# Performance work log

Hardware: AMD Instinct MI355X
Metric: run time of the kernel (lower is better)

The kernel has to match this reference:

```python
import jax, jax.numpy as jnp
import numpy as np

INPUT_DIM = 1024
EMBED_DIM = 256


def setup_inputs() -> dict:
    key = jax.random.key(0)
    ks = jax.random.split(key, 7)
    s_in = 1.0 / np.sqrt(INPUT_DIM)
    x = jax.random.normal(ks[0], (4, 2048, INPUT_DIM), dtype=jnp.float32)
    Wq = jax.random.uniform(ks[1], (INPUT_DIM, EMBED_DIM), jnp.float32, -s_in, s_in)
    bq = jax.random.uniform(ks[2], (EMBED_DIM,), jnp.float32, -s_in, s_in)
    Wk = jax.random.uniform(ks[3], (INPUT_DIM, EMBED_DIM), jnp.float32, -s_in, s_in)
    bk = jax.random.uniform(ks[4], (EMBED_DIM,), jnp.float32, -s_in, s_in)
    Wv = jax.random.uniform(ks[5], (INPUT_DIM, EMBED_DIM), jnp.float32, -s_in, s_in)
    bv = jax.random.uniform(ks[6], (EMBED_DIM,), jnp.float32, -s_in, s_in)
    return {"x": x, "Wq": Wq, "bq": bq, "Wk": Wk, "bk": bk, "Wv": Wv, "bv": bv}


def reference(x, Wq, bq, Wk, bk, Wv, bv):
    # B,T,C -> single-head attention. NOTE: original multiplies by C**0.5.
    C = x.shape[-1]
    scale = jnp.asarray(C, x.dtype) ** 0.5
    q = jnp.einsum('btc,ce->bte', x, Wq) + bq  # [B,T,E]
    k = jnp.einsum('btc,ce->bte', x, Wk) + bk
    v = jnp.einsum('btc,ce->bte', x, Wv) + bv
    wei = jnp.einsum('bqe,bke->bqk', q, k) * scale  # [B,T,T]
    wei = jax.nn.softmax(wei, axis=-1)
    # dropout p=0.0 (eval): identity
    out = jnp.einsum('bqk,bke->bqe', wei, v)  # [B,T,E]
    return out
```

## Files before the change

kernel.cpp:

```cpp
#include <hip/hip_runtime.h>
#include <math.h>

#define IDIM 1024
#define EDIM 256
#define NB 4
#define NT 2048
#define NROW 8192

typedef __attribute__((ext_vector_type(8))) short short8;
typedef __attribute__((ext_vector_type(4))) float f32x4;

#define MFMA16(A,B,C) __builtin_amdgcn_mfma_f32_16x16x32_bf16(A,B,C,0,0,0)
#define GLD16(gsrc, ldst) __builtin_amdgcn_global_load_lds( \
    (const __attribute__((address_space(1))) unsigned int*)(gsrc), \
    (__attribute__((address_space(3))) unsigned int*)(ldst), 16, 0, 0)

#define WAITV4() asm volatile("s_waitcnt vmcnt(4)" ::: "memory")
#define WAITV0() asm volatile("s_waitcnt vmcnt(0)" ::: "memory")
#define BAR() do { asm volatile("" ::: "memory"); __builtin_amdgcn_s_barrier(); \
                   asm volatile("" ::: "memory"); } while (0)

__device__ __forceinline__ unsigned short f2bf(float x){
    unsigned u = __builtin_bit_cast(unsigned, x);
    u += 0x7fffu + ((u >> 16) & 1u);
    return (unsigned short)(u >> 16);
}
__device__ __forceinline__ float bf2f(unsigned short h){
    unsigned u = ((unsigned)h) << 16;
    return __builtin_bit_cast(float, u);
}

__global__ __launch_bounds__(256) void split_w(
    const float* __restrict__ Wq, const float* __restrict__ Wk, const float* __restrict__ Wv,
    ushort* __restrict__ Wqh, ushort* __restrict__ Wql,
    ushort* __restrict__ Wkh, ushort* __restrict__ Wkl,
    ushort* __restrict__ Wvh)
{
    int u = blockIdx.x * 256 + threadIdx.x;
    int z   = u >> 15;
    int rem = u & 32767;
    int ko  = rem >> 8;
    int e   = rem & 255;
    const float* W = (z == 0) ? Wq : (z == 1) ? Wk : Wv;
    ushort* Oh = (z == 0) ? Wqh : (z == 1) ? Wkh : Wvh;
    ushort* Ol = (z == 0) ? Wql : Wkl;
    union { ushort us[8]; uint4 v; } hi, lo;
    #pragma unroll
    for (int j = 0; j < 8; ++j) {
        float wv = W[(size_t)(ko * 8 + j) * 256 + e];
        unsigned short h = f2bf(wv);
        hi.us[j] = h;
        lo.us[j] = f2bf(wv - bf2f(h));
    }
    *(uint4*)(Oh + (size_t)e * 1024 + ko * 8) = hi.v;
    if (z < 2) *(uint4*)(Ol + (size_t)e * 1024 + ko * 8) = lo.v;
}

__global__ __launch_bounds__(256) void qkv_proj(
    const float* __restrict__ X,
    const ushort* __restrict__ Whq, const ushort* __restrict__ Wlq,
    const ushort* __restrict__ Whk, const ushort* __restrict__ Wlk,
    const ushort* __restrict__ Whv,
    const float* __restrict__ bq, const float* __restrict__ bk, const float* __restrict__ bv,
    ushort* __restrict__ Qh, ushort* __restrict__ Ql,
    ushort* __restrict__ Kh, ushort* __restrict__ Kl,
    ushort* __restrict__ Vt)
{
    __shared__ ushort Ah[2][259 * 8], Al[2][259 * 8];
    __shared__ ushort Bh[2][512 * 8], Bl[2][512 * 8];

    const int tid = threadIdx.x;
    const int lane = tid & 63, w = tid >> 6;
    const int ln = tid & 15, quad = (tid >> 4) & 3;
    const int z = blockIdx.z;
    const int n0 = blockIdx.x * 128, m0 = blockIdx.y * 64;
    const ushort* Wh = (z == 0) ? Whq : (z == 1) ? Whk : Whv;
    const ushort* Wl = (z == 0) ? Wlq : Wlk;

    f32x4 acc[4][2];
    #pragma unroll
    for (int mi = 0; mi < 4; ++mi)
        #pragma unroll
        for (int ni = 0; ni < 2; ++ni) acc[mi][ni] = (f32x4){0.f, 0.f, 0.f, 0.f};

    const int am = tid >> 2, ak8 = (tid & 3) * 8;
    const int unit = (tid & 3) * 65 + am;
    const float* xp = X + (size_t)(m0 + am) * IDIM + ak8;
    const ushort* bsrc0 = Wh + (size_t)(n0 + lane) * IDIM + w * 8;
    const ushort* bsrc1 = Wh + (size_t)(n0 + 64 + lane) * IDIM + w * 8;
    const ushort* blsrc0 = Wl + (size_t)(n0 + lane) * IDIM + w * 8;
    const ushort* blsrc1 = Wl + (size_t)(n0 + 64 + lane) * IDIM + w * 8;

#define QSTAGE(pb, kk) do { \
    GLD16(bsrc0 + (kk), Bh[pb] + w * 1024); \
    GLD16(bsrc1 + (kk), Bh[pb] + w * 1024 + 512); \
    if (z < 2) { GLD16(blsrc0 + (kk), Bl[pb] + w * 1024); \
                 GLD16(blsrc1 + (kk), Bl[pb] + w * 1024 + 512); } \
    float4 a0 = *(const float4*)(xp + (kk)); \
    float4 a1 = *(const float4*)(xp + (kk) + 4); \
    float xv[8] = {a0.x, a0.y, a0.z, a0.w, a1.x, a1.y, a1.z, a1.w}; \
    union { ushort us[8]; uint4 v; } hi, lo; \
    _Pragma("unroll") \
    for (int j = 0; j < 8; ++j) { \
        unsigned short hh = f2bf(xv[j]); \
        hi.us[j] = hh; \
        lo.us[j] = f2bf(xv[j] - bf2f(hh)); \
    } \
    *(uint4*)(Ah[pb] + unit * 8) = hi.v; \
    if (z < 2) *(uint4*)(Al[pb] + unit * 8) = lo.v; \
} while (0)

#define QCOMP(cb) do { \
    short8 ah[4], al4[4]; \
    _Pragma("unroll") \
    for (int mi = 0; mi < 4; ++mi) { \
        int au = quad * 65 + mi * 16 + ln; \
        ah[mi] = *(const short8*)(Ah[cb] + au * 8); \
        if (z < 2) al4[mi] = *(const short8*)(Al[cb] + au * 8); \
    } \
    __builtin_amdgcn_s_setprio(1); \
    _Pragma("unroll") \
    for (int ni = 0; ni < 2; ++ni) { \
        int bu = quad * 128 + w * 32 + ni * 16 + ln; \
        short8 bh = *(const short8*)(Bh[cb] + bu * 8); \
        if (z < 2) { \
            short8 bl = *(const short8*)(Bl[cb] + bu * 8); \
            _Pragma("unroll") \
            for (int mi = 0; mi < 4; ++mi) { \
                acc[mi][ni] = MFMA16(ah[mi], bh, acc[mi][ni]); \
                acc[mi][ni] = MFMA16(ah[mi], bl, acc[mi][ni]); \
                acc[mi][ni] = MFMA16(al4[mi], bh, acc[mi][ni]); \
            } \
        } else { \
            _Pragma("unroll") \
            for (int mi = 0; mi < 4; ++mi) \
                acc[mi][ni] = MFMA16(ah[mi], bh, acc[mi][ni]); \
        } \
    } \
    __builtin_amdgcn_s_setprio(0); \
} while (0)

    QSTAGE(0, 0);
    __syncthreads();
    #pragma unroll 1
    for (int ks2 = 0; ks2 < 16; ++ks2) {
        QSTAGE(1, ks2 * 64 + 32);
        QCOMP(0);
        __syncthreads();
        if (ks2 < 15) QSTAGE(0, ks2 * 64 + 64);
        QCOMP(1);
        __syncthreads();
    }
#undef QSTAGE
#undef QCOMP

    if (z < 2) {
        ushort* OH = (z == 0) ? Qh : Kh;
        ushort* OL = (z == 0) ? Ql : Kl;
        const float* bias = (z == 0) ? bq : bk;
        const float scale = (z == 0) ? 46.16624130844683f : 1.0f;
        #pragma unroll
        for (int ni = 0; ni < 2; ++ni) {
            int col = n0 + w * 32 + ni * 16 + ln;
            float bb = bias[col];
            #pragma unroll
            for (int mi = 0; mi < 4; ++mi)
                #pragma unroll
                for (int r = 0; r < 4; ++r) {
                    int row = m0 + mi * 16 + quad * 4 + r;
                    float v = (acc[mi][ni][r] + bb) * scale;
                    unsigned short hh = f2bf(v);
                    OH[(size_t)row * EDIM + col] = hh;
                    OL[(size_t)row * EDIM + col] = f2bf(v - bf2f(hh));
                }
        }
    } else {
        #pragma unroll
        for (int ni = 0; ni < 2; ++ni) {
            int col = n0 + w * 32 + ni * 16 + ln;
            float bb = bv[col];
            #pragma unroll
            for (int mi = 0; mi < 4; ++mi) {
                int rowb = m0 + mi * 16 + quad * 4;
                union { ushort us[4]; uint2 v; } pk;
                #pragma unroll
                for (int r = 0; r < 4; ++r) pk.us[r] = f2bf(acc[mi][ni][r] + bb);
                *(uint2*)(Vt + (size_t)col * NROW + rowb) = pk.v;
            }
        }
    }
}

__device__ __forceinline__ void stageK(const ushort* __restrict__ Kh,
                                       const ushort* __restrict__ Kl,
                                       ushort* buf, int kv0, int kc0, int w, int lane) {
    size_t rowoff = (size_t)(kv0 + w * 16 + (lane & 15)) * EDIM + (lane >> 4) * 8 + kc0 * 32;
    GLD16(Kh + rowoff,      buf + w * 512);
    GLD16(Kh + rowoff + 32, buf + 2048 + w * 512);
    GLD16(Kl + rowoff,      buf + 4096 + w * 512);
    GLD16(Kl + rowoff + 32, buf + 6144 + w * 512);
}

__device__ __forceinline__ void stageV(const ushort* __restrict__ Vt,
                                       ushort* buf, int kv0, int vs0, int w, int lane) {
    size_t gv = (size_t)(vs0 * 64 + w * 16 + (lane & 15)) * NROW + kv0 + (lane >> 4) * 8;
    GLD16(Vt + gv,      buf + w * 1024);
    GLD16(Vt + gv + 32, buf + w * 1024 + 512);
    GLD16(Vt + gv + (size_t)64 * NROW,      buf + 4096 + w * 1024);
    GLD16(Vt + gv + (size_t)64 * NROW + 32, buf + 4096 + w * 1024 + 512);
}

__global__ __launch_bounds__(256, 2) void attn(
    const ushort* __restrict__ Qh, const ushort* __restrict__ Ql,
    const ushort* __restrict__ Kh, const ushort* __restrict__ Kl,
    const ushort* __restrict__ Vt, ushort* __restrict__ Op, float* __restrict__ mlbuf)
{
    __shared__ ushort KVbuf[3 * 8192];
    __shared__ ushort Pall[4 * 1088];

    const int tid = threadIdx.x;
    const int lane = tid & 63;
    const int ln = tid & 15, quad = (tid >> 4) & 3, w = tid >> 6;
    ushort* Pw = Pall + w * 1088;

    const int id = blockIdx.x;
    const int cls = id & 15;
    const int b = cls >> 2, kvq = cls & 3;
    const int qt = id >> 4;
    const int qrow0w = b * NT + qt * 64 + w * 16;
    const int kvbase = b * NT + kvq * 512;

    short8 qh8[8], ql8[8];
    #pragma unroll
    for (int kc = 0; kc < 8; ++kc) {
        qh8[kc] = *(const short8*)(Qh + (size_t)(qrow0w + ln) * EDIM + kc * 32 + quad * 8);
        ql8[kc] = *(const short8*)(Ql + (size_t)(qrow0w + ln) * EDIM + kc * 32 + quad * 8);
    }

    float m_r[4], l_r[4];
    #pragma unroll
    for (int r = 0; r < 4; ++r) { m_r[r] = -3e38f; l_r[r] = 0.f; }
    f32x4 o[16];
    #pragma unroll
    for (int ni = 0; ni < 16; ++ni) o[ni] = (f32x4){0.f, 0.f, 0.f, 0.f};

    stageK(Kh, Kl, KVbuf + 0 * 8192, kvbase, 0, w, lane);
    stageK(Kh, Kl, KVbuf + 1 * 8192, kvbase, 2, w, lane);

    #pragma unroll 1
    for (int t = 0; t < 8; ++t) {
        const int kv0 = kvbase + t * 64;
        f32x4 s[4];
        #pragma unroll
        for (int ni = 0; ni < 4; ++ni) s[ni] = (f32x4){0.f, 0.f, 0.f, 0.f};

        #pragma unroll
        for (int j = 0; j < 4; ++j) {
            WAITV4();
            BAR();
            if (j < 2)      stageK(Kh, Kl, KVbuf + ((j + 2) % 3) * 8192, kv0, 2 * (j + 2), w, lane);
            else if (j == 2) stageV(Vt, KVbuf + 1 * 8192, kv0, 0, w, lane);
            else             stageV(Vt, KVbuf + 2 * 8192, kv0, 2, w, lane);

            const ushort* bufc = KVbuf + (j % 3) * 8192;
            __builtin_amdgcn_s_setprio(1);
            #pragma unroll
            for (int kk = 0; kk < 2; ++kk) {
                const int kc = j * 2 + kk;
                #pragma unroll
                for (int ni = 0; ni < 4; ++ni) {
                    short8 bh = *(const short8*)(bufc + kk * 2048 + (ni * 64 + quad * 16 + ln) * 8);
                    short8 bl = *(const short8*)(bufc + 4096 + kk * 2048 + (ni * 64 + quad * 16 + ln) * 8);
                    s[ni] = MFMA16(qh8[kc], bh, s[ni]);
                    s[ni] = MFMA16(qh8[kc], bl, s[ni]);
                    s[ni] = MFMA16(ql8[kc], bh, s[ni]);
                }
            }
            __builtin_amdgcn_s_setprio(0);
        }

        float mt[4];
        #pragma unroll
        for (int r = 0; r < 4; ++r)
            mt[r] = fmaxf(fmaxf(s[0][r], s[1][r]), fmaxf(s[2][r], s[3][r]));
        #pragma unroll
        for (int mask = 1; mask < 16; mask <<= 1)
            #pragma unroll
            for (int r = 0; r < 4; ++r)
                mt[r] = fmaxf(mt[r], __shfl_xor(mt[r], mask));
        int need = (mt[0] > m_r[0]) || (mt[1] > m_r[1]) ||
                   (mt[2] > m_r[2]) || (mt[3] > m_r[3]);
        if (__ballot(need)) {
            float alpha[4];
            #pragma unroll
            for (int r = 0; r < 4; ++r) {
                float mn = fmaxf(m_r[r], mt[r]);
                alpha[r] = exp2f(m_r[r] - mn);
                m_r[r] = mn;
            }
            #pragma unroll
            for (int r = 0; r < 4; ++r) l_r[r] *= alpha[r];
            #pragma unroll
            for (int ni = 0; ni < 16; ++ni)
                #pragma unroll
                for (int r = 0; r < 4; ++r) o[ni][r] *= alpha[r];
        }
        float ls[4] = {0.f, 0.f, 0.f, 0.f};
        #pragma unroll
        for (int ni = 0; ni < 4; ++ni) {
            int colb = ni * 16 + ln;
            #pragma unroll
            for (int r = 0; r < 4; ++r) {
                float p = exp2f(s[ni][r] - m_r[r]);
                ls[r] += p;
                Pw[((colb >> 3) * 17 + quad * 4 + r) * 8 + (colb & 7)] = f2bf(p);
            }
        }
        #pragma unroll
        for (int mask = 1; mask < 16; mask <<= 1)
            #pragma unroll
            for (int r = 0; r < 4; ++r)
                ls[r] += __shfl_xor(ls[r], mask);
        #pragma unroll
        for (int r = 0; r < 4; ++r) l_r[r] += ls[r];

        short8 apk0 = *(const short8*)(Pw + (quad * 17 + ln) * 8);
        short8 apk1 = *(const short8*)(Pw + ((4 + quad) * 17 + ln) * 8);

        #pragma unroll
        for (int j2 = 0; j2 < 2; ++j2) {
            if (t < 7 || j2 == 0) { WAITV4(); } else { WAITV0(); }
            BAR();
            if (t < 7) {
                if (j2 == 0) stageK(Kh, Kl, KVbuf + 0 * 8192, kv0 + 64, 0, w, lane);
                else         stageK(Kh, Kl, KVbuf + 1 * 8192, kv0 + 64, 2, w, lane);
            }
            const ushort* bufc = KVbuf + (1 + j2) * 8192;
            __builtin_amdgcn_s_setprio(1);
            #pragma unroll
            for (int vv = 0; vv < 2; ++vv) {
                const int vs = j2 * 2 + vv;
                #pragma unroll
                for (int ni = 0; ni < 4; ++ni) {
                    short8 v0 = *(const short8*)(bufc + vv * 4096 + (ni * 128 + quad * 16 + ln) * 8);
                    short8 v1 = *(const short8*)(bufc + vv * 4096 + (ni * 128 + 64 + quad * 16 + ln) * 8);
                    o[vs * 4 + ni] = MFMA16(apk0, v0, o[vs * 4 + ni]);
                    o[vs * 4 + ni] = MFMA16(apk1, v1, o[vs * 4 + ni]);
                }
            }
            __builtin_amdgcn_s_setprio(0);
        }
    }

    const int p = (b * 32 + qt) * 4 + kvq;
    if (ln == 0) {
        #pragma unroll
        for (int r = 0; r < 4; ++r) {
            int row = w * 16 + quad * 4 + r;
            *(float2*)(mlbuf + ((size_t)p * 64 + row) * 2) = make_float2(m_r[r], l_r[r]);
        }
    }
    #pragma unroll
    for (int ni = 0; ni < 16; ++ni)
        #pragma unroll
        for (int r = 0; r < 4; ++r) {
            int row = w * 16 + quad * 4 + r;
            Op[(size_t)p * 16384 + row * 256 + ni * 16 + ln] = f2bf(o[ni][r]);
        }
}

__global__ __launch_bounds__(256) void attn_merge(
    const ushort* __restrict__ Op, const float* __restrict__ mlbuf, float* __restrict__ out)
{
    const int bid = blockIdx.x, t = threadIdx.x;
    const int b = bid >> 7, qt = (bid >> 2) & 31, rg = bid & 3;
    const int row = rg * 16 + (t >> 4);
    const int e0 = (t & 15) * 16;
    const int pb = (b * 32 + qt) * 4;
    float mv[4], lv[4];
    float M = -3e38f;
    #pragma unroll
    for (int w2 = 0; w2 < 4; ++w2) {
        float2 ml = *(const float2*)(mlbuf + ((size_t)(pb + w2) * 64 + row) * 2);
        mv[w2] = ml.x; lv[w2] = ml.y;
        M = fmaxf(M, ml.x);
    }
    float sc[4], denom = 0.f;
    #pragma unroll
    for (int w2 = 0; w2 < 4; ++w2) {
        sc[w2] = exp2f(mv[w2] - M);
        denom += sc[w2] * lv[w2];
    }
    float inv = 1.0f / denom;
    #pragma unroll
    for (int w2 = 0; w2 < 4; ++w2) sc[w2] *= inv;

    float acc[16] = {};
    #pragma unroll
    for (int w2 = 0; w2 < 4; ++w2) {
        const ushort* src = Op + (size_t)(pb + w2) * 16384 + row * 256 + e0;
        #pragma unroll
        for (int c = 0; c < 2; ++c) {
            union { ushort us[8]; uint4 v; } u;
            u.v = *(const uint4*)(src + c * 8);
            #pragma unroll
            for (int j = 0; j < 8; ++j)
                acc[c * 8 + j] += sc[w2] * bf2f(u.us[j]);
        }
    }
    float* op = out + ((size_t)b * NT + qt * 64 + row) * EDIM + e0;
    #pragma unroll
    for (int g = 0; g < 4; ++g)
        *(float4*)(op + g * 4) = make_float4(acc[g*4], acc[g*4+1], acc[g*4+2], acc[g*4+3]);
}

extern "C" void kernel_launch(void* const* d_in, const int* in_sizes, int n_in,
                              void* d_out, int out_size, void* d_ws, size_t ws_size,
                              hipStream_t stream) {
    const float* x  = (const float*)d_in[0];
    const float* Wq = (const float*)d_in[1];
    const float* bq = (const float*)d_in[2];
    const float* Wk = (const float*)d_in[3];
    const float* bk = (const float*)d_in[4];
    const float* Wv = (const float*)d_in[5];
    const float* bv = (const float*)d_in[6];
    float* out = (float*)d_out;

    const size_t NE = (size_t)NB * NT * EDIM;
    ushort* Qh = (ushort*)d_ws;
    ushort* Ql = Qh + NE;
    ushort* Kh = Ql + NE;
    ushort* Kl = Kh + NE;
    ushort* Vt = Kl + NE;
    ushort* Wqh = Vt + NE;
    ushort* Wql = Wqh + 256 * 1024;
    ushort* Wkh = Wql + 256 * 1024;
    ushort* Wkl = Wkh + 256 * 1024;
    ushort* Wvh = Wkl + 256 * 1024;
    ushort* Op  = Wvh + 256 * 1024;
    float*  mlb = (float*)(Op + (size_t)512 * 16384);

    split_w<<<384, 256, 0, stream>>>(Wq, Wk, Wv, Wqh, Wql, Wkh, Wkl, Wvh);
    qkv_proj<<<dim3(2, 128, 3), 256, 0, stream>>>(x, Wqh, Wql, Wkh, Wkl, Wvh,
                                                  bq, bk, bv, Qh, Ql, Kh, Kl, Vt);
    attn<<<512, 256, 0, stream>>>(Qh, Ql, Kh, Kl, Vt, Op, mlb);
    attn_merge<<<512, 256, 0, stream>>>(Op, mlb, out);
}
```

Baseline: 203.2 us.

## Use 128x128 tiles for Q/K projection and interleave heavy/light blocks

The QKV projection grid is restructured into a 1D grid of 512 blocks. Even blocks compute Q/K with the 3-MFMA split-bf16 scheme on 128x128 tiles, reusing each X split across twice as many rows. Odd blocks compute V with single bf16 on 64x128 tiles. Interleaving heavy and light blocks is meant to balance load across CUs and cut redundant X loading and splitting. In exchange it uses more LDS and more accumulator registers in the heavy path, which may lower occupancy.

```diff
diff --git a/kernel.cpp b/kernel.cpp
--- a/kernel.cpp
+++ b/kernel.cpp
@@ -66,38 +66,45 @@
     ushort* __restrict__ Kh, ushort* __restrict__ Kl,
     ushort* __restrict__ Vt)
 {
-    __shared__ ushort Ah[2][259 * 8], Al[2][259 * 8];
+    __shared__ ushort Ah[2][516 * 8], Al[2][516 * 8];
     __shared__ ushort Bh[2][512 * 8], Bl[2][512 * 8];
 
     const int tid = threadIdx.x;
     const int lane = tid & 63, w = tid >> 6;
     const int ln = tid & 15, quad = (tid >> 4) & 3;
-    const int z = blockIdx.z;
-    const int n0 = blockIdx.x * 128, m0 = blockIdx.y * 64;
-    const ushort* Wh = (z == 0) ? Whq : (z == 1) ? Whk : Whv;
-    const ushort* Wl = (z == 0) ? Wlq : Wlk;
-
-    f32x4 acc[4][2];
-    #pragma unroll
-    for (int mi = 0; mi < 4; ++mi)
-        #pragma unroll
-        for (int ni = 0; ni < 2; ++ni) acc[mi][ni] = (f32x4){0.f, 0.f, 0.f, 0.f};
-
-    const int am = tid >> 2, ak8 = (tid & 3) * 8;
-    const int unit = (tid & 3) * 65 + am;
-    const float* xp = X + (size_t)(m0 + am) * IDIM + ak8;
-    const ushort* bsrc0 = Wh + (size_t)(n0 + lane) * IDIM + w * 8;
-    const ushort* bsrc1 = Wh + (size_t)(n0 + 64 + lane) * IDIM + w * 8;
-    const ushort* blsrc0 = Wl + (size_t)(n0 + lane) * IDIM + w * 8;
-    const ushort* blsrc1 = Wl + (size_t)(n0 + 64 + lane) * IDIM + w * 8;
-
-#define QSTAGE(pb, kk) do { \
-    GLD16(bsrc0 + (kk), Bh[pb] + w * 1024); \
-    GLD16(bsrc1 + (kk), Bh[pb] + w * 1024 + 512); \
-    if (z < 2) { GLD16(blsrc0 + (kk), Bl[pb] + w * 1024); \
-                 GLD16(blsrc1 + (kk), Bl[pb] + w * 1024 + 512); } \
-    float4 a0 = *(const float4*)(xp + (kk)); \
-    float4 a1 = *(const float4*)(xp + (kk) + 4); \
+    const int id = blockIdx.x;
+    const bool heavy = (id & 1) == 0;
+    const int hid = id >> 1;
+
+    const int am = tid >> 2, akq = tid & 3, ak8 = akq * 8;
+
+    if (heavy) {
+        const int z = hid >> 7;
+        const int rem = hid & 127;
+        const int n0 = (rem & 1) * 128;
+        const int m0 = (rem >> 1) * 128;
+        const int wr = (w >> 1) * 64, wc = (w & 1) * 64;
+        const ushort* Wh = z ? Whk : Whq;
+        const ushort* Wl = z ? Wlk : Wlq;
+
+        f32x4 acc[4][4];
+        #pragma unroll
+        for (int mi = 0; mi < 4; ++mi)
+            #pragma unroll
+            for (int ni = 0; ni < 4; ++ni) acc[mi][ni] = (f32x4){0.f, 0.f, 0.f, 0.f};
+
+        const float* xp0 = X + (size_t)(m0 + am) * IDIM + ak8;
+        const float* xp1 = X + (size_t)(m0 + 64 + am) * IDIM + ak8;
+        const int unitA0 = akq * 129 + am;
+        const int unitA1 = akq * 129 + 64 + am;
+        const ushort* bsrc0 = Wh + (size_t)(n0 + lane) * IDIM + w * 8;
+        const ushort* bsrc1 = Wh + (size_t)(n0 + 64 + lane) * IDIM + w * 8;
+        const ushort* blsrc0 = Wl + (size_t)(n0 + lane) * IDIM + w * 8;
+        const ushort* blsrc1 = Wl + (size_t)(n0 + 64 + lane) * IDIM + w * 8;
+
+#define HSPLIT(pb, xp, unit, kk) do { \
+    float4 a0 = *(const float4*)((xp) + (kk)); \
+    float4 a1 = *(const float4*)((xp) + (kk) + 4); \
     float xv[8] = {a0.x, a0.y, a0.z, a0.w, a1.x, a1.y, a1.z, a1.w}; \
     union { ushort us[8]; uint4 v; } hi, lo; \
     _Pragma("unroll") \
@@ -106,75 +113,137 @@
         hi.us[j] = hh; \
         lo.us[j] = f2bf(xv[j] - bf2f(hh)); \
     } \
-    *(uint4*)(Ah[pb] + unit * 8) = hi.v; \
-    if (z < 2) *(uint4*)(Al[pb] + unit * 8) = lo.v; \
+    *(uint4*)(Ah[pb] + (unit) * 8) = hi.v; \
+    *(uint4*)(Al[pb] + (unit) * 8) = lo.v; \
 } while (0)
 
-#define QCOMP(cb) do { \
+#define HSTAGE(pb, kk) do { \
+    GLD16(bsrc0 + (kk), Bh[pb] + w * 1024); \
+    GLD16(bsrc1 + (kk), Bh[pb] + w * 1024 + 512); \
+    GLD16(blsrc0 + (kk), Bl[pb] + w * 1024); \
+    GLD16(blsrc1 + (kk), Bl[pb] + w * 1024 + 512); \
+    HSPLIT(pb, xp0, unitA0, kk); \
+    HSPLIT(pb, xp1, unitA1, kk); \
+} while (0)
+
+#define HCOMP(cb) do { \
     short8 ah[4], al4[4]; \
     _Pragma("unroll") \
     for (int mi = 0; mi < 4; ++mi) { \
-        int au = quad * 65 + mi * 16 + ln; \
+        int au = quad * 129 + wr + mi * 16 + ln; \
         ah[mi] = *(const short8*)(Ah[cb] + au * 8); \
-        if (z < 2) al4[mi] = *(const short8*)(Al[cb] + au * 8); \
+        al4[mi] = *(const short8*)(Al[cb] + au * 8); \
+    } \
+    __builtin_amdgcn_s_setprio(1); \
+    _Pragma("unroll") \
+    for (int ni = 0; ni < 4; ++ni) { \
+        int bu = quad * 128 + wc + ni * 16 + ln; \
+        short8 bh = *(const short8*)(Bh[cb] + bu * 8); \
+        short8 bl = *(const short8*)(Bl[cb] + bu * 8); \
+        _Pragma("unroll") \
+        for (int mi = 0; mi < 4; ++mi) { \
+            acc[mi][ni] = MFMA16(ah[mi], bh, acc[mi][ni]); \
+            acc[mi][ni] = MFMA16(ah[mi], bl, acc[mi][ni]); \
+            acc[mi][ni] = MFMA16(al4[mi], bh, acc[mi][ni]); \
+        } \
+    } \
+    __builtin_amdgcn_s_setprio(0); \
+} while (0)
+
+        HSTAGE(0, 0);
+        __syncthreads();
+        #pragma unroll 1
+        for (int ks2 = 0; ks2 < 16; ++ks2) {
+            HSTAGE(1, ks2 * 64 + 32);
+            HCOMP(0);
+            __syncthreads();
+            if (ks2 < 15) HSTAGE(0, ks2 * 64 + 64);
+            HCOMP(1);
+            __syncthreads();
+        }
+#undef HSTAGE
+#undef HSPLIT
+#undef HCOMP
+
+        ushort* OH = z ? Kh : Qh;
+        ushort* OL = z ? Kl : Ql;
+        const float* bias = z ? bk : bq;
+        const float scale = z ? 1.0f : 46.16624130844683f;
+        #pragma unroll
+        for (int ni = 0; ni < 4; ++ni) {
+            int col = n0 + wc + ni * 16 + ln;
+            float bb = bias[col];
+            #pragma unroll
+            for (int mi = 0; mi < 4; ++mi)
+                #pragma unroll
+                for (int r = 0; r < 4; ++r) {
+                    int row = m0 + wr + mi * 16 + quad * 4 + r;
+                    float v = (acc[mi][ni][r] + bb) * scale;
+                    unsigned short hh = f2bf(v);
+                    OH[(size_t)row * EDIM + col] = hh;
+                    OL[(size_t)row * EDIM + col] = f2bf(v - bf2f(hh));
+                }
+        }
+    } else {
+        const int n0 = (hid >> 7) * 128;
+        const int m0 = (hid & 127) * 64;
+
+        f32x4 acc[4][2];
+        #pragma unroll
+        for (int mi = 0; mi < 4; ++mi)
+            #pragma unroll
+            for (int ni = 0; ni < 2; ++ni) acc[mi][ni] = (f32x4){0.f, 0.f, 0.f, 0.f};
+
+        const float* xp = X + (size_t)(m0 + am) * IDIM + ak8;
+        const int unitA = akq * 129 + am;
+        const ushort* bsrc0 = Whv + (size_t)(n0 + lane) * IDIM + w * 8;
+        const ushort* bsrc1 = Whv + (size_t)(n0 + 64 + lane) * IDIM + w * 8;
+
+#define LSTAGE(pb, kk) do { \
+    GLD16(bsrc0 + (kk), Bh[pb] + w * 1024); \
+    GLD16(bsrc1 + (kk), Bh[pb] + w * 1024 + 512); \
+    float4 a0 = *(const float4*)(xp + (kk)); \
+    float4 a1 = *(const float4*)(xp + (kk) + 4); \
+    float xv[8] = {a0.x, a0.y, a0.z, a0.w, a1.x, a1.y, a1.z, a1.w}; \
+    union { ushort us[8]; uint4 v; } hi; \
+    _Pragma("unroll") \
+    for (int j = 0; j < 8; ++j) hi.us[j] = f2bf(xv[j]); \
+    *(uint4*)(Ah[pb] + unitA * 8) = hi.v; \
+} while (0)
+
+#define LCOMP(cb) do { \
+    short8 ah[4]; \
+    _Pragma("unroll") \
+    for (int mi = 0; mi < 4; ++mi) { \
+        int au = quad * 129 + mi * 16 + ln; \
+        ah[mi] = *(const short8*)(Ah[cb] + au * 8); \
     } \
     __builtin_amdgcn_s_setprio(1); \
     _Pragma("unroll") \
     for (int ni = 0; ni < 2; ++ni) { \
         int bu = quad * 128 + w * 32 + ni * 16 + ln; \
         short8 bh = *(const short8*)(Bh[cb] + bu * 8); \
-        if (z < 2) { \
-            short8 bl = *(const short8*)(Bl[cb] + bu * 8); \
-            _Pragma("unroll") \
-            for (int mi = 0; mi < 4; ++mi) { \
-                acc[mi][ni] = MFMA16(ah[mi], bh, acc[mi][ni]); \
-                acc[mi][ni] = MFMA16(ah[mi], bl, acc[mi][ni]); \
-                acc[mi][ni] = MFMA16(al4[mi], bh, acc[mi][ni]); \
-            } \
-        } else { \
-            _Pragma("unroll") \
-            for (int mi = 0; mi < 4; ++mi) \
-                acc[mi][ni] = MFMA16(ah[mi], bh, acc[mi][ni]); \
-        } \
+        _Pragma("unroll") \
+        for (int mi = 0; mi < 4; ++mi) \
+            acc[mi][ni] = MFMA16(ah[mi], bh, acc[mi][ni]); \
     } \
     __builtin_amdgcn_s_setprio(0); \
 } while (0)
 
-    QSTAGE(0, 0);
-    __syncthreads();
-    #pragma unroll 1
-    for (int ks2 = 0; ks2 < 16; ++ks2) {
-        QSTAGE(1, ks2 * 64 + 32);
-        QCOMP(0);
+        LSTAGE(0, 0);
         __syncthreads();
-        if (ks2 < 15) QSTAGE(0, ks2 * 64 + 64);
-        QCOMP(1);
-        __syncthreads();
-    }
-#undef QSTAGE
-#undef QCOMP
-
-    if (z < 2) {
-        ushort* OH = (z == 0) ? Qh : Kh;
-        ushort* OL = (z == 0) ? Ql : Kl;
-        const float* bias = (z == 0) ? bq : bk;
-        const float scale = (z == 0) ? 46.16624130844683f : 1.0f;
-        #pragma unroll
-        for (int ni = 0; ni < 2; ++ni) {
-            int col = n0 + w * 32 + ni * 16 + ln;
-            float bb = bias[col];
-            #pragma unroll
-            for (int mi = 0; mi < 4; ++mi)
-                #pragma unroll
-                for (int r = 0; r < 4; ++r) {
-                    int row = m0 + mi * 16 + quad * 4 + r;
-                    float v = (acc[mi][ni][r] + bb) * scale;
-                    unsigned short hh = f2bf(v);
-                    OH[(size_t)row * EDIM + col] = hh;
-                    OL[(size_t)row * EDIM + col] = f2bf(v - bf2f(hh));
-                }
-        }
-    } else {
+        #pragma unroll 1
+        for (int ks2 = 0; ks2 < 16; ++ks2) {
+            LSTAGE(1, ks2 * 64 + 32);
+            LCOMP(0);
+            __syncthreads();
+            if (ks2 < 15) LSTAGE(0, ks2 * 64 + 64);
+            LCOMP(1);
+            __syncthreads();
+        }
+#undef LSTAGE
+#undef LCOMP
+
         #pragma unroll
         for (int ni = 0; ni < 2; ++ni) {
             int col = n0 + w * 32 + ni * 16 + ln;
@@ -441,8 +510,8 @@
     float*  mlb = (float*)(Op + (size_t)512 * 16384);
 
     split_w<<<384, 256, 0, stream>>>(Wq, Wk, Wv, Wqh, Wql, Wkh, Wkl, Wvh);
-    qkv_proj<<<dim3(2, 128, 3), 256, 0, stream>>>(x, Wqh, Wql, Wkh, Wkl, Wvh,
-                                                  bq, bk, bv, Qh, Ql, Kh, Kl, Vt);
+    qkv_proj<<<512, 256, 0, stream>>>(x, Wqh, Wql, Wkh, Wkl, Wvh,
+                                      bq, bk, bv, Qh, Ql, Kh, Kl, Vt);
     attn<<<512, 256, 0, stream>>>(Qh, Ql, Kh, Kl, Vt, Op, mlb);
     attn_merge<<<512, 256, 0, stream>>>(Op, mlb, out);
 }
```

Result: slower. 220.1 us (+8.3%).
